# Performance work log

Hardware: AMD Instinct MI355X
Metric: run time of the kernel (lower is better)

## Reference

```python
import jax, jax.numpy as jnp
import numpy as np


def _forward(f2e_emb, score_mat, rel_features, Wk, bk,
             batch_heads, batch_rels, batch_tails, edge_mat, eps):
    B, N, D = f2e_emb.shape
    R = rel_features.shape[0]
    dt = f2e_emb.dtype
    # -cdist(x, x) then row softmax (F.softmax dim=1 on a 2D mat == last axis)
    x2 = jnp.sum(f2e_emb * f2e_emb, axis=-1)                              # [B,N]
    d2 = x2[:, :, None] + x2[:, None, :] - 2.0 * jnp.einsum('bnd,bmd->bnm', f2e_emb, f2e_emb)
    sim = jax.nn.softmax(-jnp.sqrt(jnp.maximum(d2, 0.0)), axis=-1)        # [B,N,N]
    prob = jnp.einsum('bnk,bmk->bnm', sim, score_mat)                     # sim @ score_mat.T
    cand = (prob > eps) & (edge_mat < 1)                                  # candidate (row,col) pairs
    # torch.multinomial(sim[row], 1) per candidate pair -> gumbel-max categorical,
    # one independent draw per (b, row, col) over the row's similarity distribution
    logits = jnp.log(sim)[:, :, None, :]                                  # [B,N,1,N]
    s = jax.random.categorical(jax.random.key(42),
                               jax.lax.stop_gradient(jnp.broadcast_to(logits, (B, N, N, N))),
                               axis=-1)                                    # [B,N,N]
    b3 = jnp.arange(B)[:, None, None]
    r3 = jnp.arange(N)[None, :, None]
    c3 = jnp.arange(N)[None, None, :]
    new_rel = edge_mat[b3, s, c3]                                          # [B,N,N]
    valid = (cand & (new_rel != 0)).astype(dt)
    # per-(node, relation) incidence counts: exactly equivalent to the
    # fact2head_mat/fact2tail_mat sparse.mm aggregation of kb_self_linear(rel_features[rel])
    counts = jnp.zeros((B * N * R,), dt)
    counts = counts.at[((b3 * N + r3) * R + new_rel).ravel()].add(valid.ravel())  # new edge -> head
    counts = counts.at[((b3 * N + c3) * R + new_rel).ravel()].add(valid.ravel())  # new edge -> tail
    b2 = jnp.arange(B)[:, None]
    ones = jnp.ones(batch_heads.shape, dt)
    counts = counts.at[((b2 * N + batch_heads) * R + batch_rels).ravel()].add(ones.ravel())
    counts = counts.at[((b2 * N + batch_tails) * R + batch_rels).ravel()].add(ones.ravel())
    counts = counts.reshape(B, N, R)
    Wr = rel_features @ Wk + bk                                            # kb_self_linear(rel_features) [R,O]
    return jax.nn.relu(jnp.einsum('bnr,ro->bno', counts, Wr))              # [B,N,O]


def setup_inputs():
    key = jax.random.key(0)
    ks = jax.random.split(key, 10)
    B, N, D, O, R, E = 8, 256, 256, 256, 512, 8192
    return {
        'f2e_emb': jax.random.normal(ks[0], (B, N, D), jnp.float32),
        'score_mat': jax.random.normal(ks[1], (B, N, N), jnp.float32),
        'rel_features': jax.random.normal(ks[2], (R, D), jnp.float32),
        'Wk': jax.random.normal(ks[3], (D, O), jnp.float32) / np.sqrt(D).astype(np.float32),
        'bk': jnp.zeros((O,), jnp.float32),
        'local_entity': jax.random.randint(ks[4], (B, N), 0, N, jnp.int32),
        'batch_heads': jax.random.randint(ks[5], (B, E), 0, N, jnp.int32),
        'batch_rels': jax.random.randint(ks[6], (B, E), 0, R, jnp.int32),
        'batch_tails': jax.random.randint(ks[7], (B, E), 0, N, jnp.int32),
        'edge_mat': jax.random.randint(ks[8], (B, N, N), 0, 4, jnp.int32),
        'eps': 0,
    }


def reference(f2e_emb, score_mat, rel_features, Wk, bk, local_entity,
              batch_heads, batch_rels, batch_tails, edge_mat, eps):
    return _forward(f2e_emb, score_mat, rel_features, Wk, bk,
                    batch_heads, batch_rels, batch_tails, edge_mat, eps)
```

## Files before the change

kernel.cpp:

```cpp
#include <hip/hip_runtime.h>
#include <stdint.h>

#define B 8
#define N 256
#define D 256
#define O 256
#define R 512
#define E 8192
#define TR 4
#define TRO 8
#define NSW 8192
#define F32_TINY 1.17549435e-38f

__device__ __forceinline__ void threefry2x32_k42(uint32_t x0, uint32_t x1,
                                                 uint32_t& o0, uint32_t& o1) {
  const uint32_t ks0 = 0u;
  const uint32_t ks1 = 42u;
  const uint32_t ks2 = 0u ^ 42u ^ 0x1BD11BDAu;
  x0 += ks0; x1 += ks1;
#define TF_R(r) { x0 += x1; x1 = (x1 << (r)) | (x1 >> (32 - (r))); x1 ^= x0; }
  TF_R(13) TF_R(15) TF_R(26) TF_R(6)
  x0 += ks1; x1 += ks2 + 1u;
  TF_R(17) TF_R(29) TF_R(16) TF_R(24)
  x0 += ks2; x1 += ks0 + 2u;
  TF_R(13) TF_R(15) TF_R(26) TF_R(6)
  x0 += ks0; x1 += ks1 + 3u;
  TF_R(17) TF_R(29) TF_R(16) TF_R(24)
  x0 += ks1; x1 += ks2 + 4u;
  TF_R(13) TF_R(15) TF_R(26) TF_R(6)
  x0 += ks2; x1 += ks0 + 5u;
#undef TF_R
  o0 = x0; o1 = x1;
}

__device__ __forceinline__ float gumbel_from_bits_f(float f) {
  float u = (f == 0.0f) ? F32_TINY : f;
  return -logf(-logf(u));
}

__global__ __launch_bounds__(256) void prep_kernel(const float* __restrict__ score,
                                                   float* __restrict__ scoreT,
                                                   const float* __restrict__ f2e,
                                                   float* __restrict__ f2eT,
                                                   const float* __restrict__ relf,
                                                   const float* __restrict__ Wk,
                                                   const float* __restrict__ bk,
                                                   float* __restrict__ Wr,
                                                   int* __restrict__ wcount) {
  int blk = blockIdx.x;
  if (blk == 0 && threadIdx.x == 0) *wcount = 0;
  if (blk < 256) {
    __shared__ float tile[64][65];
    const float* src = (blk < 128) ? score : f2e;
    float* dst = (blk < 128) ? scoreT : f2eT;
    int b7 = blk & 127;
    int bb = b7 >> 4, t = b7 & 15, ti = t >> 2, tj = t & 3;
    size_t base = (size_t)bb * 65536;
    int c = threadIdx.x & 63, r4 = threadIdx.x >> 6;
#pragma unroll
    for (int rr = 0; rr < 64; rr += 4) {
      int row = rr + r4;
      tile[row][c] = src[base + (size_t)(ti * 64 + row) * 256 + tj * 64 + c];
    }
    __syncthreads();
#pragma unroll
    for (int rr = 0; rr < 64; rr += 4) {
      int row = rr + r4;
      dst[base + (size_t)(tj * 64 + row) * 256 + ti * 64 + c] = tile[c][row];
    }
  } else {
    __shared__ float rrow[TR][D];
    int r0 = (blk - 256) * TR;
    int o = threadIdx.x;
#pragma unroll
    for (int r = 0; r < TR; ++r) rrow[r][o] = relf[(size_t)(r0 + r) * D + o];
    __syncthreads();
    double acc[TR] = {0, 0, 0, 0};
    for (int d = 0; d < D; d += 4) {
      float w0 = Wk[(size_t)(d + 0) * O + o];
      float w1 = Wk[(size_t)(d + 1) * O + o];
      float w2 = Wk[(size_t)(d + 2) * O + o];
      float w3 = Wk[(size_t)(d + 3) * O + o];
#pragma unroll
      for (int r = 0; r < TR; ++r) {
        float4 a = *(const float4*)&rrow[r][d];
        acc[r] += (double)a.x * w0; acc[r] += (double)a.y * w1;
        acc[r] += (double)a.z * w2; acc[r] += (double)a.w * w3;
      }
    }
    float bv = bk[o];
#pragma unroll
    for (int r = 0; r < TR; ++r) Wr[(size_t)(r0 + r) * O + o] = (float)acc[r] + bv;
  }
}

__global__ __launch_bounds__(256) void simcand_kernel(const float* __restrict__ f2e,
                                                      const float* __restrict__ f2eT,
                                                      const float* __restrict__ scoreT,
                                                      const int* __restrict__ edge,
                                                      const int* __restrict__ epsp,
                                                      float* __restrict__ logits,
                                                      float* __restrict__ laux,
                                                      int* __restrict__ wlist,
                                                      int* __restrict__ wcount) {
  int bn0 = blockIdx.x * TR;
  int b = bn0 >> 8;
  int tid = threadIdx.x, lane = tid & 63, w = tid >> 6;
  __shared__ float arow[TR][256];
  __shared__ float nbuf[TR][256];
  __shared__ float x2s[256];
#pragma unroll
  for (int r = 0; r < TR; ++r) arow[r][tid] = f2e[(size_t)(bn0 + r) * 256 + tid];
  __syncthreads();
  double acc[TR] = {0, 0, 0, 0};
  double ax2 = 0.0;
  const float* fT = f2eT + (size_t)b * 65536 + tid;
  for (int dd = 0; dd < 256; dd += 4) {
    float b0 = fT[(size_t)(dd + 0) * 256];
    float b1 = fT[(size_t)(dd + 1) * 256];
    float b2 = fT[(size_t)(dd + 2) * 256];
    float b3 = fT[(size_t)(dd + 3) * 256];
    ax2 += (double)b0 * b0; ax2 += (double)b1 * b1;
    ax2 += (double)b2 * b2; ax2 += (double)b3 * b3;
#pragma unroll
    for (int r = 0; r < TR; ++r) {
      float4 a = *(const float4*)&arow[r][dd];
      acc[r] += (double)a.x * b0; acc[r] += (double)a.y * b1;
      acc[r] += (double)a.z * b2; acc[r] += (double)a.w * b3;
    }
  }
  float x2c = (float)ax2;
  x2s[tid] = x2c;
  __syncthreads();
#pragma unroll
  for (int r = 0; r < TR; ++r) {
    float x2r = x2s[(bn0 + r) & 255];
    float d2 = (x2r + x2c) - 2.0f * (float)acc[r];
    nbuf[r][tid] = -sqrtf(fmaxf(d2, 0.0f));
  }
  __syncthreads();
  {
    float v0 = nbuf[w][lane], v1 = nbuf[w][lane + 64],
          v2 = nbuf[w][lane + 128], v3 = nbuf[w][lane + 192];
    float mx = fmaxf(fmaxf(v0, v1), fmaxf(v2, v3));
#pragma unroll
    for (int off = 32; off > 0; off >>= 1) mx = fmaxf(mx, __shfl_xor(mx, off));
    float p0 = expf(v0 - mx), p1 = expf(v1 - mx), p2 = expf(v2 - mx), p3 = expf(v3 - mx);
    double sd = (double)p0 + (double)p1 + (double)p2 + (double)p3;
#pragma unroll
    for (int off = 32; off > 0; off >>= 1) sd += __shfl_xor(sd, off);
    float denom = (float)sd;
    float s0 = p0 / denom, s1 = p1 / denom, s2 = p2 / denom, s3 = p3 / denom;
    arow[w][lane] = s0; arow[w][lane + 64] = s1;
    arow[w][lane + 128] = s2; arow[w][lane + 192] = s3;
    float l0 = logf(s0), l1 = logf(s1), l2 = logf(s2), l3 = logf(s3);
    size_t rb = (size_t)(bn0 + w) * 256;
    logits[rb + lane] = l0; logits[rb + lane + 64] = l1;
    logits[rb + lane + 128] = l2; logits[rb + lane + 192] = l3;
    int dm = (bn0 + w) & 255;
    int dj = dm >> 6, dl = dm & 63;
    float e0 = (dj == 0 && lane == dl) ? -3.4e38f : l0;
    float e1 = (dj == 1 && lane == dl) ? -3.4e38f : l1;
    float e2 = (dj == 2 && lane == dl) ? -3.4e38f : l2;
    float e3 = (dj == 3 && lane == dl) ? -3.4e38f : l3;
    float Lm = fmaxf(fmaxf(e0, e1), fmaxf(e2, e3));
#pragma unroll
    for (int off = 32; off > 0; off >>= 1) Lm = fmaxf(Lm, __shfl_xor(Lm, off));
    float lown = (dj == 0) ? l0 : (dj == 1) ? l1 : (dj == 2) ? l2 : l3;
    float l_n = __shfl(lown, dl);
    if (lane == 0) {
      laux[2 * (bn0 + w) + 0] = l_n;
      laux[2 * (bn0 + w) + 1] = Lm;
    }
  }
  __syncthreads();
  double acc2[TR] = {0, 0, 0, 0};
  const float* sT = scoreT + (size_t)b * 65536 + tid;
  for (int kk = 0; kk < 256; kk += 4) {
    float b0 = sT[(size_t)(kk + 0) * 256];
    float b1 = sT[(size_t)(kk + 1) * 256];
    float b2 = sT[(size_t)(kk + 2) * 256];
    float b3 = sT[(size_t)(kk + 3) * 256];
#pragma unroll
    for (int r = 0; r < TR; ++r) {
      float4 a = *(const float4*)&arow[r][kk];
      acc2[r] += (double)a.x * b0; acc2[r] += (double)a.y * b1;
      acc2[r] += (double)a.z * b2; acc2[r] += (double)a.w * b3;
    }
  }
  float epsv = (float)epsp[0];
#pragma unroll
  for (int r = 0; r < TR; ++r) {
    int row = (bn0 + r) * 256 + tid;
    int em = edge[(size_t)row];
    bool active = ((float)acc2[r] > epsv) && (em < 1);
    unsigned long long mask = __ballot(active);
    int cnt = __popcll(mask);
    int basev = 0;
    if (lane == 0 && cnt) basev = atomicAdd(wcount, cnt);
    basev = __shfl(basev, 0);
    if (active) {
      int pos = basev + __popcll(mask & ((1ull << lane) - 1ull));
      wlist[pos] = row;
    }
  }
}

__global__ __launch_bounds__(256) void sample_kernel(const float* __restrict__ logits,
                                                     const float* __restrict__ laux,
                                                     const int* __restrict__ wlist,
                                                     const int* __restrict__ wcount,
                                                     const int* __restrict__ edge,
                                                     const int* __restrict__ heads,
                                                     const int* __restrict__ rels,
                                                     const int* __restrict__ tails,
                                                     float* __restrict__ counts) {
  int blk = blockIdx.x;
  if (blk >= 2048) {
    int i = (blk - 2048) * 256 + threadIdx.x;
    int b = i >> 13;
    int h = heads[i], r = rels[i], t = tails[i];
    atomicAdd(&counts[(size_t)(b * N + h) * R + r], 1.0f);
    atomicAdd(&counts[(size_t)(b * N + t) * R + r], 1.0f);
    return;
  }
  int lane = threadIdx.x & 63;
  int gw = blk * 4 + (threadIdx.x >> 6);
  int cnt = *wcount;
  for (int idx = gw; idx < cnt; idx += NSW) {
    int row = wlist[idx];
    int b = row >> 16;
    int n = (row >> 8) & 255;
    int c = row & 255;
    uint32_t base = (uint32_t)row << 8;
    float u0, u1, u2, u3;
    {
      uint32_t a0, a1;
#define GEN_U(q, dst)                                                     \
      threefry2x32_k42(0u, base + (uint32_t)((q) * 64 + lane), a0, a1);    \
      dst = __uint_as_float((((a0 ^ a1) >> 9)) | 0x3f800000u) - 1.0f;
      GEN_U(0, u0) GEN_U(1, u1) GEN_U(2, u2) GEN_U(3, u3)
#undef GEN_U
    }
    float l_n  = laux[2 * ((b << 8) + n) + 0];
    float Lmax = laux[2 * ((b << 8) + n) + 1];
    int qo = n >> 6;
    float uo = (qo == 0) ? u0 : (qo == 1) ? u1 : (qo == 2) ? u2 : u3;
    float u_n = __shfl(uo, n & 63);
    float v_n = gumbel_from_bits_f(u_n) + l_n;
    float thr_g = (v_n - Lmax) - 0.125f;
    float u_thr = expf(-expf(-thr_g));
    bool owner = (lane == (n & 63));
    bool anyc = ((u0 > u_thr) && !(owner && qo == 0)) |
                ((u1 > u_thr) && !(owner && qo == 1)) |
                ((u2 > u_thr) && !(owner && qo == 2)) |
                ((u3 > u_thr) && !(owner && qo == 3));
    if (!__any(anyc)) continue;

    const float* lrow = logits + (size_t)((b << 8) + n) * N;
    float bestv = -1e30f;
    int besti = 0;
    for (int q = 0; q < 4; ++q) {
      int k = q * 64 + lane;
      uint32_t o0, o1;
      threefry2x32_k42(0u, base + (uint32_t)k, o0, o1);
      uint32_t bits = o0 ^ o1;
      float f = __uint_as_float((bits >> 9) | 0x3f800000u) - 1.0f;
      float g = gumbel_from_bits_f(f);
      float v = g + lrow[k];
      if (v > bestv || (v == bestv && k < besti)) { bestv = v; besti = k; }
    }
    for (int off = 32; off > 0; off >>= 1) {
      float ov = __shfl_down(bestv, off);
      int oi = __shfl_down(besti, off);
      if (ov > bestv || (ov == bestv && oi < besti)) { bestv = ov; besti = oi; }
    }
    if (lane == 0) {
      int nr = edge[(size_t)((b << 8) + besti) * N + c];
      if (nr != 0) {
        atomicAdd(&counts[(size_t)((b << 8) + n) * R + nr], 1.0f);
        atomicAdd(&counts[(size_t)((b << 8) + c) * R + nr], 1.0f);
      }
    }
  }
}

__global__ __launch_bounds__(256) void out_kernel(const float* __restrict__ counts,
                                                  const float* __restrict__ Wr,
                                                  float* __restrict__ out) {
  int bn0 = blockIdx.x * TRO;
  int o = threadIdx.x;
  __shared__ float crow[TRO][R];
#pragma unroll
  for (int r = 0; r < TRO; ++r) {
    crow[r][o] = counts[(size_t)(bn0 + r) * R + o];
    crow[r][o + 256] = counts[(size_t)(bn0 + r) * R + 256 + o];
  }
  __syncthreads();
  float acc[TRO] = {0, 0, 0, 0, 0, 0, 0, 0};
  for (int k = 0; k < R; k += 4) {
    float w0 = Wr[(size_t)(k + 0) * O + o];
    float w1 = Wr[(size_t)(k + 1) * O + o];
    float w2 = Wr[(size_t)(k + 2) * O + o];
    float w3 = Wr[(size_t)(k + 3) * O + o];
#pragma unroll
    for (int r = 0; r < TRO; ++r) {
      float4 cv = *(const float4*)&crow[r][k];
      acc[r] += cv.x * w0; acc[r] += cv.y * w1;
      acc[r] += cv.z * w2; acc[r] += cv.w * w3;
    }
  }
#pragma unroll
  for (int r = 0; r < TRO; ++r)
    out[(size_t)(bn0 + r) * O + o] = fmaxf(acc[r], 0.0f);
}

extern "C" void kernel_launch(void* const* d_in, const int* in_sizes, int n_in,
                              void* d_out, int out_size, void* d_ws, size_t ws_size,
                              hipStream_t stream) {
  (void)in_sizes; (void)n_in; (void)out_size; (void)ws_size;
  const float* f2e   = (const float*)d_in[0];
  const float* score = (const float*)d_in[1];
  const float* relf  = (const float*)d_in[2];
  const float* Wk    = (const float*)d_in[3];
  const float* bk    = (const float*)d_in[4];
  const int* heads   = (const int*)d_in[6];
  const int* rels    = (const int*)d_in[7];
  const int* tails   = (const int*)d_in[8];
  const int* edge    = (const int*)d_in[9];
  const int* epsp    = (const int*)d_in[10];
  float* out = (float*)d_out;

  float* ws     = (float*)d_ws;
  float* logits = ws;
  float* Wr     = logits + 524288;
  float* counts = Wr + 131072;
  float* scoreT = counts;
  float* f2eT   = counts + 524288;
  float* laux   = counts + 1048576;
  int*   wlist  = (int*)(laux + 4096);
  int*   wcount = wlist + 524288;

  prep_kernel<<<384, 256, 0, stream>>>(score, scoreT, f2e, f2eT,
                                       relf, Wk, bk, Wr, wcount);
  simcand_kernel<<<(B * N) / TR, 256, 0, stream>>>(f2e, f2eT, scoreT, edge, epsp,
                                                   logits, laux, wlist, wcount);
  hipMemsetAsync(counts, 0, (size_t)B * N * R * sizeof(float), stream);
  sample_kernel<<<2048 + 256, 256, 0, stream>>>(logits, laux, wlist, wcount, edge,
                                                heads, rels, tails, counts);
  out_kernel<<<(B * N) / TRO, 256, 0, stream>>>(counts, Wr, out);
}
```

Measured before the change: 214.1 us.

## Switch FP64 accumulators to split FP32 and split sim/candidate kernels

Replaces the double-precision dot-product accumulation in the Wr projection, the pairwise distance GEMM and the sim@score product with two interleaved FP32 accumulators. Row norms are precomputed once in extra prep blocks instead of being recomputed per block. The fused sim+candidate kernel is split into two kernels, and sim is written to global memory as the handoff. FP64 throughput is the main cost being targeted. The trade is an extra launch plus an extra sim write and read, and a precision risk for the threshold and sampling decisions.

Result: no change. 217.4 us (+1.6%).

```diff
diff --git a/kernel.cpp b/kernel.cpp
--- a/kernel.cpp
+++ b/kernel.cpp
@@ -46,9 +46,11 @@
                                                    const float* __restrict__ Wk,
                                                    const float* __restrict__ bk,
                                                    float* __restrict__ Wr,
+                                                   float* __restrict__ x2,
                                                    int* __restrict__ wcount) {
   int blk = blockIdx.x;
-  if (blk == 0 && threadIdx.x == 0) *wcount = 0;
+  int tid = threadIdx.x;
+  if (blk == 0 && tid == 0) *wcount = 0;
   if (blk < 256) {
     __shared__ float tile[64][65];
     const float* src = (blk < 128) ? score : f2e;
@@ -56,7 +58,7 @@
     int b7 = blk & 127;
     int bb = b7 >> 4, t = b7 & 15, ti = t >> 2, tj = t & 3;
     size_t base = (size_t)bb * 65536;
-    int c = threadIdx.x & 63, r4 = threadIdx.x >> 6;
+    int c = tid & 63, r4 = tid >> 6;
 #pragma unroll
     for (int rr = 0; rr < 64; rr += 4) {
       int row = rr + r4;
@@ -68,14 +70,14 @@
       int row = rr + r4;
       dst[base + (size_t)(tj * 64 + row) * 256 + ti * 64 + c] = tile[c][row];
     }
-  } else {
+  } else if (blk < 384) {
     __shared__ float rrow[TR][D];
     int r0 = (blk - 256) * TR;
-    int o = threadIdx.x;
+    int o = tid;
 #pragma unroll
     for (int r = 0; r < TR; ++r) rrow[r][o] = relf[(size_t)(r0 + r) * D + o];
     __syncthreads();
-    double acc[TR] = {0, 0, 0, 0};
+    float accA[TR] = {0, 0, 0, 0}, accB[TR] = {0, 0, 0, 0};
     for (int d = 0; d < D; d += 4) {
       float w0 = Wk[(size_t)(d + 0) * O + o];
       float w1 = Wk[(size_t)(d + 1) * O + o];
@@ -84,97 +86,110 @@
 #pragma unroll
       for (int r = 0; r < TR; ++r) {
         float4 a = *(const float4*)&rrow[r][d];
-        acc[r] += (double)a.x * w0; acc[r] += (double)a.y * w1;
-        acc[r] += (double)a.z * w2; acc[r] += (double)a.w * w3;
+        accA[r] += a.x * w0; accB[r] += a.y * w1;
+        accA[r] += a.z * w2; accB[r] += a.w * w3;
       }
     }
     float bv = bk[o];
 #pragma unroll
-    for (int r = 0; r < TR; ++r) Wr[(size_t)(r0 + r) * O + o] = (float)acc[r] + bv;
-  }
-}
-
-__global__ __launch_bounds__(256) void simcand_kernel(const float* __restrict__ f2e,
-                                                      const float* __restrict__ f2eT,
-                                                      const float* __restrict__ scoreT,
-                                                      const int* __restrict__ edge,
-                                                      const int* __restrict__ epsp,
-                                                      float* __restrict__ logits,
-                                                      float* __restrict__ laux,
-                                                      int* __restrict__ wlist,
-                                                      int* __restrict__ wcount) {
+    for (int r = 0; r < TR; ++r)
+      Wr[(size_t)(r0 + r) * O + o] = (accA[r] + accB[r]) + bv;
+  } else {
+    int i = (blk - 384) * 256 + tid;
+    const float4* p = (const float4*)(f2e + (size_t)i * D);
+    double s = 0.0;
+    for (int d = 0; d < D / 4; ++d) {
+      float4 v = p[d];
+      s += (double)v.x * v.x; s += (double)v.y * v.y;
+      s += (double)v.z * v.z; s += (double)v.w * v.w;
+    }
+    x2[i] = (float)s;
+  }
+}
+
+__global__ __launch_bounds__(256) void sim_kernel(const float* __restrict__ f2e,
+                                                  const float* __restrict__ f2eT,
+                                                  const float* __restrict__ x2,
+                                                  float* __restrict__ sim,
+                                                  float* __restrict__ logits,
+                                                  float* __restrict__ laux) {
   int bn0 = blockIdx.x * TR;
   int b = bn0 >> 8;
   int tid = threadIdx.x, lane = tid & 63, w = tid >> 6;
   __shared__ float arow[TR][256];
   __shared__ float nbuf[TR][256];
-  __shared__ float x2s[256];
 #pragma unroll
   for (int r = 0; r < TR; ++r) arow[r][tid] = f2e[(size_t)(bn0 + r) * 256 + tid];
   __syncthreads();
-  double acc[TR] = {0, 0, 0, 0};
-  double ax2 = 0.0;
+  float aA[TR] = {0, 0, 0, 0}, aB[TR] = {0, 0, 0, 0};
   const float* fT = f2eT + (size_t)b * 65536 + tid;
   for (int dd = 0; dd < 256; dd += 4) {
     float b0 = fT[(size_t)(dd + 0) * 256];
     float b1 = fT[(size_t)(dd + 1) * 256];
     float b2 = fT[(size_t)(dd + 2) * 256];
     float b3 = fT[(size_t)(dd + 3) * 256];
-    ax2 += (double)b0 * b0; ax2 += (double)b1 * b1;
-    ax2 += (double)b2 * b2; ax2 += (double)b3 * b3;
 #pragma unroll
     for (int r = 0; r < TR; ++r) {
       float4 a = *(const float4*)&arow[r][dd];
-      acc[r] += (double)a.x * b0; acc[r] += (double)a.y * b1;
-      acc[r] += (double)a.z * b2; acc[r] += (double)a.w * b3;
-    }
-  }
-  float x2c = (float)ax2;
-  x2s[tid] = x2c;
+      aA[r] += a.x * b0; aB[r] += a.y * b1;
+      aA[r] += a.z * b2; aB[r] += a.w * b3;
+    }
+  }
+  float x2c = x2[b * 256 + tid];
+#pragma unroll
+  for (int r = 0; r < TR; ++r) {
+    float d2 = (x2[bn0 + r] + x2c) - 2.0f * (aA[r] + aB[r]);
+    nbuf[r][tid] = -sqrtf(fmaxf(d2, 0.0f));
+  }
   __syncthreads();
-#pragma unroll
-  for (int r = 0; r < TR; ++r) {
-    float x2r = x2s[(bn0 + r) & 255];
-    float d2 = (x2r + x2c) - 2.0f * (float)acc[r];
-    nbuf[r][tid] = -sqrtf(fmaxf(d2, 0.0f));
-  }
+  float v0 = nbuf[w][lane], v1 = nbuf[w][lane + 64],
+        v2 = nbuf[w][lane + 128], v3 = nbuf[w][lane + 192];
+  float mx = fmaxf(fmaxf(v0, v1), fmaxf(v2, v3));
+#pragma unroll
+  for (int off = 32; off > 0; off >>= 1) mx = fmaxf(mx, __shfl_xor(mx, off));
+  float p0 = expf(v0 - mx), p1 = expf(v1 - mx), p2 = expf(v2 - mx), p3 = expf(v3 - mx);
+  double sd = (double)p0 + (double)p1 + (double)p2 + (double)p3;
+#pragma unroll
+  for (int off = 32; off > 0; off >>= 1) sd += __shfl_xor(sd, off);
+  float denom = (float)sd;
+  float s0 = p0 / denom, s1 = p1 / denom, s2 = p2 / denom, s3 = p3 / denom;
+  size_t rb = (size_t)(bn0 + w) * 256;
+  sim[rb + lane] = s0; sim[rb + lane + 64] = s1;
+  sim[rb + lane + 128] = s2; sim[rb + lane + 192] = s3;
+  float l0 = logf(s0), l1 = logf(s1), l2 = logf(s2), l3 = logf(s3);
+  logits[rb + lane] = l0; logits[rb + lane + 64] = l1;
+  logits[rb + lane + 128] = l2; logits[rb + lane + 192] = l3;
+  int dm = (bn0 + w) & 255;
+  int dj = dm >> 6, dl = dm & 63;
+  float e0 = (dj == 0 && lane == dl) ? -3.4e38f : l0;
+  float e1 = (dj == 1 && lane == dl) ? -3.4e38f : l1;
+  float e2 = (dj == 2 && lane == dl) ? -3.4e38f : l2;
+  float e3 = (dj == 3 && lane == dl) ? -3.4e38f : l3;
+  float Lm = fmaxf(fmaxf(e0, e1), fmaxf(e2, e3));
+#pragma unroll
+  for (int off = 32; off > 0; off >>= 1) Lm = fmaxf(Lm, __shfl_xor(Lm, off));
+  float lown = (dj == 0) ? l0 : (dj == 1) ? l1 : (dj == 2) ? l2 : l3;
+  float l_n = __shfl(lown, dl);
+  if (lane == 0) {
+    laux[2 * (bn0 + w) + 0] = l_n;
+    laux[2 * (bn0 + w) + 1] = Lm;
+  }
+}
+
+__global__ __launch_bounds__(256) void cand_kernel(const float* __restrict__ sim,
+                                                   const float* __restrict__ scoreT,
+                                                   const int* __restrict__ edge,
+                                                   const int* __restrict__ epsp,
+                                                   int* __restrict__ wlist,
+                                                   int* __restrict__ wcount) {
+  int bn0 = blockIdx.x * TR;
+  int b = bn0 >> 8;
+  int tid = threadIdx.x, lane = tid & 63;
+  __shared__ float srow[TR][256];
+#pragma unroll
+  for (int r = 0; r < TR; ++r) srow[r][tid] = sim[(size_t)(bn0 + r) * 256 + tid];
   __syncthreads();
-  {
-    float v0 = nbuf[w][lane], v1 = nbuf[w][lane + 64],
-          v2 = nbuf[w][lane + 128], v3 = nbuf[w][lane + 192];
-    float mx = fmaxf(fmaxf(v0, v1), fmaxf(v2, v3));
-#pragma unroll
-    for (int off = 32; off > 0; off >>= 1) mx = fmaxf(mx, __shfl_xor(mx, off));
-    float p0 = expf(v0 - mx), p1 = expf(v1 - mx), p2 = expf(v2 - mx), p3 = expf(v3 - mx);
-    double sd = (double)p0 + (double)p1 + (double)p2 + (double)p3;
-#pragma unroll
-    for (int off = 32; off > 0; off >>= 1) sd += __shfl_xor(sd, off);
-    float denom = (float)sd;
-    float s0 = p0 / denom, s1 = p1 / denom, s2 = p2 / denom, s3 = p3 / denom;
-    arow[w][lane] = s0; arow[w][lane + 64] = s1;
-    arow[w][lane + 128] = s2; arow[w][lane + 192] = s3;
-    float l0 = logf(s0), l1 = logf(s1), l2 = logf(s2), l3 = logf(s3);
-    size_t rb = (size_t)(bn0 + w) * 256;
-    logits[rb + lane] = l0; logits[rb + lane + 64] = l1;
-    logits[rb + lane + 128] = l2; logits[rb + lane + 192] = l3;
-    int dm = (bn0 + w) & 255;
-    int dj = dm >> 6, dl = dm & 63;
-    float e0 = (dj == 0 && lane == dl) ? -3.4e38f : l0;
-    float e1 = (dj == 1 && lane == dl) ? -3.4e38f : l1;
-    float e2 = (dj == 2 && lane == dl) ? -3.4e38f : l2;
-    float e3 = (dj == 3 && lane == dl) ? -3.4e38f : l3;
-    float Lm = fmaxf(fmaxf(e0, e1), fmaxf(e2, e3));
-#pragma unroll
-    for (int off = 32; off > 0; off >>= 1) Lm = fmaxf(Lm, __shfl_xor(Lm, off));
-    float lown = (dj == 0) ? l0 : (dj == 1) ? l1 : (dj == 2) ? l2 : l3;
-    float l_n = __shfl(lown, dl);
-    if (lane == 0) {
-      laux[2 * (bn0 + w) + 0] = l_n;
-      laux[2 * (bn0 + w) + 1] = Lm;
-    }
-  }
-  __syncthreads();
-  double acc2[TR] = {0, 0, 0, 0};
+  float aA[TR] = {0, 0, 0, 0}, aB[TR] = {0, 0, 0, 0};
   const float* sT = scoreT + (size_t)b * 65536 + tid;
   for (int kk = 0; kk < 256; kk += 4) {
     float b0 = sT[(size_t)(kk + 0) * 256];
@@ -183,9 +198,9 @@
     float b3 = sT[(size_t)(kk + 3) * 256];
 #pragma unroll
     for (int r = 0; r < TR; ++r) {
-      float4 a = *(const float4*)&arow[r][kk];
-      acc2[r] += (double)a.x * b0; acc2[r] += (double)a.y * b1;
-      acc2[r] += (double)a.z * b2; acc2[r] += (double)a.w * b3;
+      float4 a = *(const float4*)&srow[r][kk];
+      aA[r] += a.x * b0; aB[r] += a.y * b1;
+      aA[r] += a.z * b2; aB[r] += a.w * b3;
     }
   }
   float epsv = (float)epsp[0];
@@ -193,7 +208,7 @@
   for (int r = 0; r < TR; ++r) {
     int row = (bn0 + r) * 256 + tid;
     int em = edge[(size_t)row];
-    bool active = ((float)acc2[r] > epsv) && (em < 1);
+    bool active = ((aA[r] + aB[r]) > epsv) && (em < 1);
     unsigned long long mask = __ballot(active);
     int cnt = __popcll(mask);
     int basev = 0;
@@ -333,18 +348,20 @@
 
   float* ws     = (float*)d_ws;
   float* logits = ws;
-  float* Wr     = logits + 524288;
+  float* sim    = logits + 524288;
+  float* Wr     = sim + 524288;
   float* counts = Wr + 131072;
   float* scoreT = counts;
   float* f2eT   = counts + 524288;
   float* laux   = counts + 1048576;
-  int*   wlist  = (int*)(laux + 4096);
+  float* x2     = laux + 4096;
+  int*   wlist  = (int*)(x2 + 2048);
   int*   wcount = wlist + 524288;
 
-  prep_kernel<<<384, 256, 0, stream>>>(score, scoreT, f2e, f2eT,
-                                       relf, Wk, bk, Wr, wcount);
-  simcand_kernel<<<(B * N) / TR, 256, 0, stream>>>(f2e, f2eT, scoreT, edge, epsp,
-                                                   logits, laux, wlist, wcount);
+  prep_kernel<<<392, 256, 0, stream>>>(score, scoreT, f2e, f2eT,
+                                       relf, Wk, bk, Wr, x2, wcount);
+  sim_kernel<<<(B * N) / TR, 256, 0, stream>>>(f2e, f2eT, x2, sim, logits, laux);
+  cand_kernel<<<(B * N) / TR, 256, 0, stream>>>(sim, scoreT, edge, epsp, wlist, wcount);
   hipMemsetAsync(counts, 0, (size_t)B * N * R * sizeof(float), stream);
   sample_kernel<<<2048 + 256, 256, 0, stream>>>(logits, laux, wlist, wcount, edge,
                                                 heads, rels, tails, counts);
```
